# Optimization experiments

Measured on AMD Instinct MI355X. Metric: run time of the kernel, lower is better.

The kernel has to match this reference:

```python
import jax, jax.numpy as jnp
import numpy as np

B, C, N = 8, 256, 1024
D, DK, DV, H, NB = 256, 16, 32, 8, 4
P = N + 1


def layernorm(x, g, b, eps=1e-5):
    m = x.mean(-1, keepdims=True)
    v = x.var(-1, keepdims=True)
    return (x - m) / jnp.sqrt(v + eps) * g + b


def bn_inf(x, g, b, mean, var, eps=1e-5):
    # x: [B, C', N]; stats over channel dim
    scale = (g / jnp.sqrt(var + eps))[None, :, None]
    shift = (b - mean * g / jnp.sqrt(var + eps))[None, :, None]
    return x * scale + shift


def softmax_with_policy(attn, policy, eps=1e-6):
    # attn: [B,H,P,P], policy: [B,P,1]
    n = attn.shape[-1]
    ap = policy.reshape(policy.shape[0], 1, 1, n)
    eye = jnp.eye(n, dtype=ap.dtype)[None, None]
    ap = ap + (1.0 - ap) * eye
    m = attn.max(-1, keepdims=True)
    e = jnp.exp(attn - m) * ap
    return (e + eps / n) / (e.sum(-1, keepdims=True) + eps)


def setup_inputs() -> dict:
    key = jax.random.key(0)
    ks = jax.random.split(key, 24)
    s = 0.02
    inp = {
        'x': jax.random.normal(ks[0], (B, C, N), jnp.float32),
        'policy': jnp.ones((B, P, 1), jnp.float32),
        'conv1_w': jax.random.normal(ks[1], (D, C), jnp.float32) * s,
        'conv2_w': jax.random.normal(ks[2], (D, D), jnp.float32) * s,
        'bn1_g': jnp.ones((D,), jnp.float32),
        'bn1_b': jnp.zeros((D,), jnp.float32),
        'bn1_m': jax.random.normal(ks[3], (D,), jnp.float32) * s,
        'bn1_v': jax.random.uniform(ks[4], (D,), jnp.float32, 0.5, 1.5),
        'bn2_g': jnp.ones((D,), jnp.float32),
        'bn2_b': jnp.zeros((D,), jnp.float32),
        'bn2_m': jax.random.normal(ks[5], (D,), jnp.float32) * s,
        'bn2_v': jax.random.uniform(ks[6], (D,), jnp.float32, 0.5, 1.5),
        'cls_token': jax.random.normal(ks[7], (D,), jnp.float32),
        'ln1_g': jnp.ones((NB, D), jnp.float32),
        'ln1_b': jnp.zeros((NB, D), jnp.float32),
        'ln2_g': jnp.ones((NB, D), jnp.float32),
        'ln2_b': jnp.zeros((NB, D), jnp.float32),
        'wq': jax.random.normal(ks[8], (NB, H * DK, D), jnp.float32) * np.sqrt(2.0 / (D + DK)).astype(np.float32),
        'wk': jax.random.normal(ks[9], (NB, H * DK, D), jnp.float32) * np.sqrt(2.0 / (D + DK)).astype(np.float32),
        'wv': jax.random.normal(ks[10], (NB, H * DV, D), jnp.float32) * np.sqrt(2.0 / (D + DV)).astype(np.float32),
        'fc_w': jax.random.normal(ks[11], (NB, D, H * DV), jnp.float32) * s,
        'ff_w1': jax.random.normal(ks[12], (NB, 2 * D, D), jnp.float32) * s,
        'ff_b1': jnp.zeros((NB, 2 * D), jnp.float32),
        'ff_w2': jax.random.normal(ks[13], (NB, D, 2 * D), jnp.float32) * s,
        'ff_b2': jnp.zeros((NB, D), jnp.float32),
    }
    return inp


def reference(x, policy, conv1_w, conv2_w, bn1_g, bn1_b, bn1_m, bn1_v,
              bn2_g, bn2_b, bn2_m, bn2_v, cls_token,
              ln1_g, ln1_b, ln2_g, ln2_b, wq, wk, wv, fc_w,
              ff_w1, ff_b1, ff_w2, ff_b2):
    # stem: 1x1 conv + BN(inference) + ReLU, twice. x: [B, C, N]
    h = jax.nn.relu(bn_inf(jnp.einsum('dc,bcn->bdn', conv1_w, x), bn1_g, bn1_b, bn1_m, bn1_v))
    h = jax.nn.relu(bn_inf(jnp.einsum('dc,bcn->bdn', conv2_w, h), bn2_g, bn2_b, bn2_m, bn2_v))
    h = h.transpose(0, 2, 1)  # [B, N, D]
    cls = jnp.broadcast_to(cls_token[None, None, :], (B, 1, D))
    h = jnp.concatenate([cls, h], axis=1)  # [B, P, D]

    scale = 1.0 / np.sqrt(DK).astype(np.float32)
    for i in range(NB):
        # attention
        y = layernorm(h, ln1_g[i], ln1_b[i])
        q = jnp.einsum('bnd,ed->bne', y, wq[i]).reshape(B, P, H, DK).transpose(0, 2, 1, 3)
        k = jnp.einsum('bnd,ed->bne', y, wk[i]).reshape(B, P, H, DK).transpose(0, 2, 1, 3)
        v = jnp.einsum('bnd,ed->bne', y, wv[i]).reshape(B, P, H, DV).transpose(0, 2, 1, 3)
        attn = jnp.einsum('bhlk,bhtk->bhlt', q, k) * scale
        attn = softmax_with_policy(attn, policy)
        o = jnp.einsum('bhlt,bhtv->bhlv', attn, v)  # [B,H,P,DV]
        o = o.transpose(0, 2, 1, 3).reshape(B, P, H * DV)
        h = h + jnp.einsum('bne,de->bnd', o, fc_w[i])
        # feed-forward
        y = layernorm(h, ln2_g[i], ln2_b[i])
        y = jax.nn.gelu(jnp.einsum('bnd,ed->bne', y, ff_w1[i]) + ff_b1[i], approximate=False)
        h = h + jnp.einsum('bne,de->bnd', y, ff_w2[i]) + ff_b2[i]
    return h
```

## Files before the change

kernel.cpp:

```cpp
#include <hip/hip_runtime.h>
#include <stdint.h>


typedef unsigned short u16;
typedef unsigned int   u32;
typedef __bf16 bf16x8 __attribute__((ext_vector_type(8)));
typedef float  f32x4  __attribute__((ext_vector_type(4)));
typedef float  f32x16 __attribute__((ext_vector_type(16)));
typedef u32    u32x4  __attribute__((ext_vector_type(4)));

#define DEV static __device__ __forceinline__

DEV float b2f(u16 h){ u32 u = ((u32)h) << 16; return __builtin_bit_cast(float, u); }
DEV u16 f2b(float f){ u32 u = __builtin_bit_cast(u32, f); u32 r = (u + 0x7fffu + ((u >> 16) & 1u)) >> 16; return (u16)r; }
DEV float gelu_f(float x){ return 0.5f * x * (1.0f + erff(x * 0.7071067811865475f)); }
DEV u32 cvtpk(float lo, float hi){
  u32 w;
  asm("v_cvt_pk_bf16_f32 %0, %1, %2" : "=v"(w) : "v"(lo), "v"(hi));
  return w;
}
DEV float exp2_(float x){ float r; asm("v_exp_f32 %0, %1" : "=v"(r) : "v"(x)); return r; }

typedef void __attribute__((address_space(1)))* gas_t;
typedef void __attribute__((address_space(3)))* las_t;
DEV void cp16(const void* g, void* l){
  __builtin_amdgcn_global_load_lds((gas_t)(uintptr_t)g, (las_t)(uintptr_t)l, 16, 0, 0);
}

struct Seg { const float* src; u16* dst; int n; int period; int dstride; int block0; float scale; };
struct SegPack { Seg s[8]; };

__global__ __launch_bounds__(256) void k_convert(SegPack p){
  int bid = blockIdx.x;
  int si = 0;
  #pragma unroll
  for (int i = 1; i < 8; i++) if (bid >= p.s[i].block0) si = i;
  const Seg sg = p.s[si];
  int e0 = (bid - sg.block0) * 2048 + threadIdx.x * 8;
  #pragma unroll
  for (int k = 0; k < 8; k++){
    int e = e0 + k;
    if (e < sg.n) sg.dst[(e / sg.period) * sg.dstride + (e % sg.period)] = f2b(sg.src[e] * sg.scale);
  }
}

__global__ __launch_bounds__(256) void k_transpose_x(const float* __restrict__ x, u16* __restrict__ xT){
  __shared__ float t[32][33];
  int b = blockIdx.z, ct = blockIdx.y, nt = blockIdx.x;
  int tx = threadIdx.x & 31, ty = threadIdx.x >> 5;
  const float* xp = x + ((size_t)b * 256 + ct * 32) * 1024 + nt * 32;
  #pragma unroll
  for (int k = 0; k < 4; k++) t[ty + 8*k][tx] = xp[(size_t)(ty + 8*k) * 1024 + tx];
  __syncthreads();
  u16* op = xT + ((size_t)b * 1024 + nt * 32) * 256 + ct * 32;
  #pragma unroll
  for (int k = 0; k < 4; k++) op[(size_t)(ty + 8*k) * 256 + tx] = f2b(t[tx][ty + 8*k]);
}

__global__ void k_cls(const float* __restrict__ cls, float* __restrict__ h){
  int d = threadIdx.x;
  #pragma unroll
  for (int b = 0; b < 8; b++) h[(size_t)b * 1025 * 256 + d] = cls[d];
}

__global__ __launch_bounds__(256) void k_ln(const float* __restrict__ h, const float* __restrict__ g,
                                            const float* __restrict__ bt, u16* __restrict__ y){
  int lane = threadIdx.x & 63, wv = threadIdx.x >> 6;
  long t = (long)blockIdx.x * 4 + wv;
  if (t >= 8200) return;
  const float* row = h + t * 256;
  float4 v = *reinterpret_cast<const float4*>(row + lane * 4);
  float s = v.x + v.y + v.z + v.w;
  float q = v.x*v.x + v.y*v.y + v.z*v.z + v.w*v.w;
  #pragma unroll
  for (int o = 32; o > 0; o >>= 1){ s += __shfl_xor(s, o); q += __shfl_xor(q, o); }
  float mean = s * (1.f/256.f);
  float var  = q * (1.f/256.f) - mean * mean;
  float rs = rsqrtf(var + 1e-5f);
  ushort4 ov;
  const float* vp = &v.x;
  u16* o16 = (u16*)&ov;
  #pragma unroll
  for (int j = 0; j < 4; j++){
    int c = lane * 4 + j;
    o16[j] = f2b((vp[j] - mean) * rs * g[c] + bt[c]);
  }
  *reinterpret_cast<ushort4*>(y + t * 256 + lane * 4) = ov;
}

template<int EPI, int BM, int BN>
__global__ __launch_bounds__(256) void k_gemmT(const u16* __restrict__ A, const u16* __restrict__ W,
    int M, int K, int E, float* __restrict__ outF, u16* __restrict__ outB,
    u16* __restrict__ outK,
    const float* __restrict__ a0, const float* __restrict__ a1,
    const float* __restrict__ a2, const float* __restrict__ a3){
  constexpr int MR = BM / 32, NR = BN / 32;
  __shared__ __align__(16) u16 As[BM * 64];
  __shared__ __align__(16) u16 Bs[BN * 64];
  const int MTILES = (M + BM - 1) / BM;
  const int MT8 = (MTILES + 7) >> 3;
  const int bid = blockIdx.x;
  const int xcd = bid & 7, rest = bid >> 3;
  const int mi = xcd + 8 * (rest % MT8);
  const int ni = rest / MT8;
  if (mi >= MTILES) return;
  const int tM = mi * BM, tN = ni * BN;
  const int tid = threadIdx.x;
  const int lane = tid & 63, wv = tid >> 6;
  const int wr = wv >> 1, wc = wv & 1;
  f32x4 acc[MR][NR];
  #pragma unroll
  for (int m = 0; m < MR; m++)
    #pragma unroll
    for (int n = 0; n < NR; n++)
      #pragma unroll
      for (int j = 0; j < 4; j++) acc[m][n][j] = 0.f;

  const int l8 = lane >> 3, lm = lane & 7;
  for (int k0 = 0; k0 < K; k0 += 64){
    __syncthreads();
    #pragma unroll
    for (int is = 0; is < BM / 32; is++){
      int row = is * 32 + wv * 8 + l8;
      int kg = lm ^ (row & 7);
      int ra = tM + row; ra = ra < M ? ra : M - 1;
      cp16(A + (size_t)ra * K + k0 + kg * 8, As + is * 2048 + wv * 512);
    }
    #pragma unroll
    for (int is = 0; is < BN / 32; is++){
      int row = is * 32 + wv * 8 + l8;
      int kg = lm ^ (row & 7);
      cp16(W + (size_t)(tN + row) * K + k0 + kg * 8, Bs + is * 2048 + wv * 512);
    }
    __syncthreads();
    #pragma unroll
    for (int kk = 0; kk < 2; kk++){
      bf16x8 af[MR], bfv[NR];
      #pragma unroll
      for (int m = 0; m < MR; m++){
        int row = wr * (BM/2) + m * 16 + (lane & 15);
        int kg = (kk * 4 + (lane >> 4)) ^ (row & 7);
        af[m] = *reinterpret_cast<const bf16x8*>(&As[row * 64 + kg * 8]);
      }
      #pragma unroll
      for (int n = 0; n < NR; n++){
        int row = wc * (BN/2) + n * 16 + (lane & 15);
        int kg = (kk * 4 + (lane >> 4)) ^ (row & 7);
        bfv[n] = *reinterpret_cast<const bf16x8*>(&Bs[row * 64 + kg * 8]);
      }
      #pragma unroll
      for (int m = 0; m < MR; m++)
        #pragma unroll
        for (int n = 0; n < NR; n++)
          acc[m][n] = __builtin_amdgcn_mfma_f32_16x16x32_bf16(af[m], bfv[n], acc[m][n], 0, 0, 0);
    }
  }
  #pragma unroll
  for (int n = 0; n < NR; n++){
    const int col = tN + wc * (BN/2) + n * 16 + (lane & 15);
    float scale = 0.f, shift = 0.f, bias = 0.f;
    if (EPI == 1 || EPI == 2){
      float gv = a0[col], bv = a1[col], mv = a2[col], vv = a3[col];
      scale = gv * rsqrtf(vv + 1e-5f);
      shift = bv - mv * scale;
    }
    if (EPI == 4 || EPI == 5) bias = a0[col];
    #pragma unroll
    for (int m = 0; m < MR; m++){
      const int row0 = tM + wr * (BM/2) + m * 16 + ((lane >> 4) << 2);
      #pragma unroll
      for (int j = 0; j < 4; j++){
        int r = row0 + j;
        if (r < M){
          float v = acc[m][n][j];
          if (EPI == 1){ v = v * scale + shift; v = v > 0.f ? v : 0.f; outB[(size_t)r * E + col] = f2b(v); }
          else if (EPI == 2){ v = v * scale + shift; v = v > 0.f ? v : 0.f; outF[(size_t)(r + (r >> 10) + 1) * 256 + col] = v; }
          else if (EPI == 3){ outF[(size_t)r * E + col] += v; }
          else if (EPI == 4){ outB[(size_t)r * E + col] = f2b(gelu_f(v + bias)); }
          else if (EPI == 5){ outF[(size_t)r * E + col] += v + bias; }
          else {
            int bb = r / 1025, tok = r - bb * 1025;
            if (col < 128){
              outB[(size_t)r * 512 + col] = f2b(v);
            } else if (col < 256){
              int hk = (col - 128) >> 4, dk = col & 15;
              outK[((size_t)((bb * 8 + hk) * 1032 + tok)) * 16 + dk] = f2b(v);
            } else {
              u16 bv = f2b(v);
              outB[(size_t)r * 512 + col] = bv;
              u16* vt = (u16*)outF;
              int hv = (col - 256) >> 5, dv = (col - 256) & 31;
              vt[((size_t)((bb * 8 + hv) * 32 + dv)) * 1032 + tok] = bv;
            }
          }
        }
      }
    }
  }
}

__global__ __launch_bounds__(256) void k_attn(const u16* __restrict__ qkv,
    const u16* __restrict__ kb, const u16* __restrict__ vt,
    const float* __restrict__ pol, u16* __restrict__ o){
  __shared__ float pol_s[1088];
  __shared__ float oB[3][32][33];
  __shared__ float lsB[3][32];
  const int tid = threadIdx.x;
  const int lane = tid & 63, wv = tid >> 6;
  const int l32 = lane & 31, hi = lane >> 5;
  const int bid = blockIdx.x;
  const int xcd = bid & 7, idx = bid >> 3;
  const int bh = xcd * 8 + idx / 33, qt = idx % 33;
  const int b = bh >> 3, hh = bh & 7;
  const size_t rowbase = (size_t)b * 1025;
  const u16* kbh = kb + (size_t)bh * 1032 * 16;
  const int qg = qt * 32 + l32;
  const int qr = qg > 1024 ? 1024 : qg;
  const bf16x8 qf = *reinterpret_cast<const bf16x8*>(qkv + (rowbase + qr) * 512 + hh * 16 + hi * 8);
  float sqq = 0.f, scl = 0.f;
  {
    const bf16x8 kown = *reinterpret_cast<const bf16x8*>(kbh + (size_t)qr * 16 + hi * 8);
    const bf16x8 kcls = *reinterpret_cast<const bf16x8*>(kbh + (size_t)1024 * 16 + hi * 8);
    #pragma unroll
    for (int i = 0; i < 8; i++){
      sqq += (float)qf[i] * (float)kown[i];
      scl += (float)qf[i] * (float)kcls[i];
    }
    sqq += __shfl_xor(sqq, 32);
    scl += __shfl_xor(scl, 32);
  }
  const u16* vrow = vt + ((size_t)(bh * 32 + l32)) * 1032;
  const u16* krow = kbh + (size_t)((wv * 256) + l32) * 16 + hi * 8;
  for (int t = tid; t < 1088; t += 256){
    float p = (t <= 1024) ? pol[rowbase + t] : 0.f;
    pol_s[t] = (p > 0.f) ? __log2f(p) : -1.0e30f;
  }
  __syncthreads();

  float ls = 0.f;
  f32x16 oacc;
  #pragma unroll
  for (int r = 0; r < 16; r++) oacc[r] = 0.f;

  bf16x8 ka = *reinterpret_cast<const bf16x8*>(krow);
  #pragma unroll
  for (int s8 = 0; s8 < 8; s8++){
    const int jb32 = wv * 256 + s8 * 32;
    const bf16x8 ka_cur = ka;
    if (s8 < 7) ka = *reinterpret_cast<const bf16x8*>(krow + (size_t)(s8 + 1) * 512);
    const bf16x8 va0 = *reinterpret_cast<const bf16x8*>(vrow + jb32 + hi * 8);
    const bf16x8 va1 = *reinterpret_cast<const bf16x8*>(vrow + jb32 + 16 + hi * 8);
    f32x16 fz;
    #pragma unroll
    for (int r = 0; r < 16; r++) fz[r] = 0.f;
    f32x16 st = __builtin_amdgcn_mfma_f32_32x32x16_bf16(ka_cur, qf, fz, 0, 0, 0);
    float e[16];
    #pragma unroll
    for (int r = 0; r < 16; r++){
      int jg2 = jb32 + (r & 3) + 8 * (r >> 2) + 4 * hi;
      e[r] = exp2_(st[r] + pol_s[jg2]);
    }
    float s01 = (e[0] + e[1]) + (e[2] + e[3]);
    float s23 = (e[4] + e[5]) + (e[6] + e[7]);
    float s45 = (e[8] + e[9]) + (e[10] + e[11]);
    float s67 = (e[12] + e[13]) + (e[14] + e[15]);
    float psum = (s01 + s23) + (s45 + s67);
    psum += __shfl_xor(psum, 32);
    ls += psum;
    #pragma unroll
    for (int c = 0; c < 2; c++){
      u32 A0 = cvtpk(e[c*8+0], e[c*8+1]);
      u32 A1 = cvtpk(e[c*8+2], e[c*8+3]);
      u32 B0 = cvtpk(e[c*8+4], e[c*8+5]);
      u32 B1 = cvtpk(e[c*8+6], e[c*8+7]);
      u32 pA0 = __shfl_xor(A0, 32), pB0 = __shfl_xor(B0, 32);
      u32 pA1 = __shfl_xor(A1, 32), pB1 = __shfl_xor(B1, 32);
      u32x4 pw;
      pw.x = hi ? pB0 : A0;
      pw.y = hi ? pB1 : A1;
      pw.z = hi ? B0 : pA0;
      pw.w = hi ? B1 : pA1;
      bf16x8 pb = __builtin_bit_cast(bf16x8, pw);
      oacc = __builtin_amdgcn_mfma_f32_32x32x16_bf16(c == 0 ? va0 : va1, pb, oacc, 0, 0, 0);
    }
  }
  __syncthreads();
  if (wv > 0){
    lsB[wv-1][l32] = ls;
    #pragma unroll
    for (int r = 0; r < 16; r++) oB[wv-1][l32][(r & 3) + 8 * (r >> 2) + 4 * hi] = oacc[r];
  }
  __syncthreads();
  if (wv == 0 && qg <= 1024){
    float ls_t = (ls + lsB[0][l32]) + (lsB[1][l32] + lsB[2][l32]);
    const float pq = exp2_(pol_s[qg]);
    const float ec = (1.f - pq) * exp2_(sqq);
    const float ecl = exp2_(scl + pol_s[1024]);
    ls_t += ec + ecl;
    const float inv = 1.f / (ls_t + 1e-6f);
    u16* orow = o + (rowbase + qg) * 256 + hh * 32;
    const u16* vq   = qkv + (rowbase + qg) * 512 + 256 + hh * 32;
    const u16* vcls = qkv + (rowbase + 1024) * 512 + 256 + hh * 32;
    #pragma unroll
    for (int rq = 0; rq < 4; rq++){
      const int dv0 = 8 * rq + 4 * hi;
      const ushort4 vv4 = *reinterpret_cast<const ushort4*>(vq + dv0);
      const ushort4 vc4 = *reinterpret_cast<const ushort4*>(vcls + dv0);
      const u16* vv = (const u16*)&vv4;
      const u16* vc = (const u16*)&vc4;
      uint2 wout;
      u32* wp = &wout.x;
      #pragma unroll
      for (int j2 = 0; j2 < 2; j2++){
        const int d0 = dv0 + j2 * 2;
        float v0 = (oacc[rq*4 + j2*2    ] + oB[0][l32][d0    ] + oB[1][l32][d0    ] + oB[2][l32][d0    ]
                    + ec * b2f(vv[j2*2    ]) + ecl * b2f(vc[j2*2    ])) * inv;
        float v1 = (oacc[rq*4 + j2*2 + 1] + oB[0][l32][d0 + 1] + oB[1][l32][d0 + 1] + oB[2][l32][d0 + 1]
                    + ec * b2f(vv[j2*2 + 1]) + ecl * b2f(vc[j2*2 + 1])) * inv;
        wp[j2] = ((u32)f2b(v1) << 16) | (u32)f2b(v0);
      }
      *reinterpret_cast<uint2*>(orow + dv0) = wout;
    }
  }
}

extern "C" void kernel_launch(void* const* d_in, const int* in_sizes, int n_in,
                              void* d_out, int out_size, void* d_ws, size_t ws_size,
                              hipStream_t stream){
  const float* x    = (const float*)d_in[0];
  const float* pol  = (const float*)d_in[1];
  const float* c1w  = (const float*)d_in[2];
  const float* c2w  = (const float*)d_in[3];
  const float* bn1g = (const float*)d_in[4];
  const float* bn1b = (const float*)d_in[5];
  const float* bn1m = (const float*)d_in[6];
  const float* bn1v = (const float*)d_in[7];
  const float* bn2g = (const float*)d_in[8];
  const float* bn2b = (const float*)d_in[9];
  const float* bn2m = (const float*)d_in[10];
  const float* bn2v = (const float*)d_in[11];
  const float* cls  = (const float*)d_in[12];
  const float* ln1g = (const float*)d_in[13];
  const float* ln1b = (const float*)d_in[14];
  const float* ln2g = (const float*)d_in[15];
  const float* ln2b = (const float*)d_in[16];
  const float* wq   = (const float*)d_in[17];
  const float* wk   = (const float*)d_in[18];
  const float* wvp  = (const float*)d_in[19];
  const float* fcw  = (const float*)d_in[20];
  const float* ffw1 = (const float*)d_in[21];
  const float* ffb1 = (const float*)d_in[22];
  const float* ffw2 = (const float*)d_in[23];
  const float* ffb2 = (const float*)d_in[24];
  float* h = (float*)d_out;

  u16* ws   = (u16*)d_ws;
  u16* wc1  = ws;
  u16* wc2  = wc1  + 65536;
  u16* wqkv = wc2  + 65536;
  u16* wfc  = wqkv + 524288;
  u16* wff1 = wfc  + 262144;
  u16* wff2 = wff1 + 524288;
  u16* xT   = wff2 + 524288;
  u16* h1   = xT   + 2097152;
  u16* yb   = h1   + 2097152;
  u16* qkvb = yb   + 2099200;
  u16* ob   = qkvb + 4198400;
  u16* vtb  = ob   + 2099200;
  u16* kbb  = vtb  + 2117632;
  u16* ub   = qkvb;

  const float QSCALE = 0.25f * 1.4426950408889634f;
  SegPack sp;
  int b0 = 0;
  sp.s[0] = Seg{ c1w,  wc1,          65536,  65536,  0,      b0, 1.f }; b0 += 32;
  sp.s[1] = Seg{ c2w,  wc2,          65536,  65536,  0,      b0, 1.f }; b0 += 32;
  sp.s[2] = Seg{ wq,   wqkv,         131072, 32768,  131072, b0, QSCALE }; b0 += 64;
  sp.s[3] = Seg{ wk,   wqkv + 32768, 131072, 32768,  131072, b0, 1.f }; b0 += 64;
  sp.s[4] = Seg{ wvp,  wqkv + 65536, 262144, 65536,  131072, b0, 1.f }; b0 += 128;
  sp.s[5] = Seg{ fcw,  wfc,          262144, 262144, 0,      b0, 1.f }; b0 += 128;
  sp.s[6] = Seg{ ffw1, wff1,         524288, 524288, 0,      b0, 1.f }; b0 += 256;
  sp.s[7] = Seg{ ffw2, wff2,         524288, 524288, 0,      b0, 1.f }; b0 += 256;

  k_convert<<<b0, 256, 0, stream>>>(sp);
  k_transpose_x<<<dim3(32, 8, 8), 256, 0, stream>>>(x, xT);
  k_cls<<<1, 256, 0, stream>>>(cls, h);
  k_gemmT<1,64,64><<<8*16*4, 256, 0, stream>>>(xT, wc1, 8192, 256, 256, nullptr, h1, nullptr,
                                               bn1g, bn1b, bn1m, bn1v);
  k_gemmT<2,64,64><<<8*16*4, 256, 0, stream>>>(h1, wc2, 8192, 256, 256, h, nullptr, nullptr,
                                               bn2g, bn2b, bn2m, bn2v);
  for (int i = 0; i < 4; i++){
    k_ln<<<2050, 256, 0, stream>>>(h, ln1g + i*256, ln1b + i*256, yb);
    k_gemmT<6,64,128><<<8*17*4, 256, 0, stream>>>(yb, wqkv + i*131072, 8200, 256, 512,
                                                  (float*)vtb, qkvb, kbb,
                                                  nullptr, nullptr, nullptr, nullptr);
    k_attn<<<2112, 256, 0, stream>>>(qkvb, kbb, vtb, pol, ob);
    k_gemmT<3,64,64><<<8*17*4, 256, 0, stream>>>(ob, wfc + i*65536, 8200, 256, 256, h, nullptr, nullptr,
                                                 nullptr, nullptr, nullptr, nullptr);
    k_ln<<<2050, 256, 0, stream>>>(h, ln2g + i*256, ln2b + i*256, yb);
    k_gemmT<4,64,128><<<8*17*4, 256, 0, stream>>>(yb, wff1 + i*131072, 8200, 256, 512, nullptr, ub, nullptr,
                                                  ffb1 + i*512, nullptr, nullptr, nullptr);
    k_gemmT<5,64,64><<<8*17*4, 256, 0, stream>>>(ub, wff2 + i*131072, 8200, 512, 256, h, nullptr, nullptr,
                                                 ffb2 + i*256, nullptr, nullptr, nullptr);
  }
}
```

Before: 354.8 us.

## Fuse layernorm into the QKV and FF1 GEMM prologues

Removes the standalone layernorm kernel. A new GEMM kernel loads the whole 64x256 fp32 activation tile, normalises it in registers, and stores it once as bf16 in a swizzled LDS tile before the K loop. Only the weight tiles are then streamed. This drops eight launches and the bf16 y round-trip through global memory. In exchange, each N-tile block (four per row tile) recomputes the layernorm and rereads fp32 h, and the larger LDS footprint may reduce occupancy.

```diff
diff --git a/kernel.cpp b/kernel.cpp
--- a/kernel.cpp
+++ b/kernel.cpp
@@ -63,35 +63,9 @@
   for (int b = 0; b < 8; b++) h[(size_t)b * 1025 * 256 + d] = cls[d];
 }
 
-__global__ __launch_bounds__(256) void k_ln(const float* __restrict__ h, const float* __restrict__ g,
-                                            const float* __restrict__ bt, u16* __restrict__ y){
-  int lane = threadIdx.x & 63, wv = threadIdx.x >> 6;
-  long t = (long)blockIdx.x * 4 + wv;
-  if (t >= 8200) return;
-  const float* row = h + t * 256;
-  float4 v = *reinterpret_cast<const float4*>(row + lane * 4);
-  float s = v.x + v.y + v.z + v.w;
-  float q = v.x*v.x + v.y*v.y + v.z*v.z + v.w*v.w;
-  #pragma unroll
-  for (int o = 32; o > 0; o >>= 1){ s += __shfl_xor(s, o); q += __shfl_xor(q, o); }
-  float mean = s * (1.f/256.f);
-  float var  = q * (1.f/256.f) - mean * mean;
-  float rs = rsqrtf(var + 1e-5f);
-  ushort4 ov;
-  const float* vp = &v.x;
-  u16* o16 = (u16*)&ov;
-  #pragma unroll
-  for (int j = 0; j < 4; j++){
-    int c = lane * 4 + j;
-    o16[j] = f2b((vp[j] - mean) * rs * g[c] + bt[c]);
-  }
-  *reinterpret_cast<ushort4*>(y + t * 256 + lane * 4) = ov;
-}
-
 template<int EPI, int BM, int BN>
 __global__ __launch_bounds__(256) void k_gemmT(const u16* __restrict__ A, const u16* __restrict__ W,
     int M, int K, int E, float* __restrict__ outF, u16* __restrict__ outB,
-    u16* __restrict__ outK,
     const float* __restrict__ a0, const float* __restrict__ a1,
     const float* __restrict__ a2, const float* __restrict__ a3){
   constexpr int MR = BM / 32, NR = BN / 32;
@@ -164,7 +138,7 @@
       scale = gv * rsqrtf(vv + 1e-5f);
       shift = bv - mv * scale;
     }
-    if (EPI == 4 || EPI == 5) bias = a0[col];
+    if (EPI == 5) bias = a0[col];
     #pragma unroll
     for (int m = 0; m < MR; m++){
       const int row0 = tM + wr * (BM/2) + m * 16 + ((lane >> 4) << 2);
@@ -176,8 +150,126 @@
           if (EPI == 1){ v = v * scale + shift; v = v > 0.f ? v : 0.f; outB[(size_t)r * E + col] = f2b(v); }
           else if (EPI == 2){ v = v * scale + shift; v = v > 0.f ? v : 0.f; outF[(size_t)(r + (r >> 10) + 1) * 256 + col] = v; }
           else if (EPI == 3){ outF[(size_t)r * E + col] += v; }
-          else if (EPI == 4){ outB[(size_t)r * E + col] = f2b(gelu_f(v + bias)); }
-          else if (EPI == 5){ outF[(size_t)r * E + col] += v + bias; }
+          else { outF[(size_t)r * E + col] += v + bias; }
+        }
+      }
+    }
+  }
+}
+
+template<int EPI>
+__global__ __launch_bounds__(256) void k_gln(const float* __restrict__ hA, const u16* __restrict__ W,
+    int M, int E, const float* __restrict__ lg, const float* __restrict__ lb,
+    float* __restrict__ outF, u16* __restrict__ outB, u16* __restrict__ outK,
+    const float* __restrict__ a0){
+  constexpr int BM = 64, BN = 128, MR = 2, NR = 4;
+  __shared__ __align__(16) u16 As[64 * 256];
+  __shared__ __align__(16) u16 Bs[BN * 64];
+  const int MTILES = (M + BM - 1) / BM;
+  const int MT8 = (MTILES + 7) >> 3;
+  const int bid = blockIdx.x;
+  const int xcd = bid & 7, rest = bid >> 3;
+  const int mi = xcd + 8 * (rest % MT8);
+  const int ni = rest / MT8;
+  if (mi >= MTILES) return;
+  const int tM = mi * BM, tN = ni * BN;
+  const int tid = threadIdx.x;
+  const int lane = tid & 63, wv = tid >> 6;
+  const int wr = wv >> 1, wc = wv & 1;
+
+  {
+    const int r = tid >> 2, qd = tid & 3;
+    int ra = tM + r; ra = ra < M ? ra : M - 1;
+    const float* hrow = hA + (size_t)ra * 256 + qd * 64;
+    float4 hv[16];
+    #pragma unroll
+    for (int c = 0; c < 16; c++) hv[c] = *reinterpret_cast<const float4*>(hrow + c * 4);
+    float s = 0.f, q = 0.f;
+    #pragma unroll
+    for (int c = 0; c < 16; c++){
+      s += (hv[c].x + hv[c].y) + (hv[c].z + hv[c].w);
+      q += (hv[c].x*hv[c].x + hv[c].y*hv[c].y) + (hv[c].z*hv[c].z + hv[c].w*hv[c].w);
+    }
+    s += __shfl_xor(s, 1); s += __shfl_xor(s, 2);
+    q += __shfl_xor(q, 1); q += __shfl_xor(q, 2);
+    const float mean = s * (1.f/256.f);
+    const float var  = q * (1.f/256.f) - mean * mean;
+    const float rs = rsqrtf(var + 1e-5f);
+    #pragma unroll
+    for (int w = 0; w < 8; w++){
+      u32x4 d;
+      #pragma unroll
+      for (int half = 0; half < 2; half++){
+        const int c = 2 * w + half;
+        const float4 g4 = *reinterpret_cast<const float4*>(lg + qd * 64 + c * 4);
+        const float4 b4 = *reinterpret_cast<const float4*>(lb + qd * 64 + c * 4);
+        float v0 = (hv[c].x - mean) * rs * g4.x + b4.x;
+        float v1 = (hv[c].y - mean) * rs * g4.y + b4.y;
+        float v2 = (hv[c].z - mean) * rs * g4.z + b4.z;
+        float v3 = (hv[c].w - mean) * rs * g4.w + b4.w;
+        d[half*2 + 0] = cvtpk(v0, v1);
+        d[half*2 + 1] = cvtpk(v2, v3);
+      }
+      const int gL = (qd * 8 + w) ^ (r & 7);
+      *reinterpret_cast<u32x4*>(&As[r * 256 + gL * 8]) = d;
+    }
+  }
+
+  f32x4 acc[MR][NR];
+  #pragma unroll
+  for (int m = 0; m < MR; m++)
+    #pragma unroll
+    for (int n = 0; n < NR; n++)
+      #pragma unroll
+      for (int j = 0; j < 4; j++) acc[m][n][j] = 0.f;
+
+  const int l8 = lane >> 3, lm = lane & 7;
+  for (int k0 = 0; k0 < 256; k0 += 64){
+    __syncthreads();
+    #pragma unroll
+    for (int is = 0; is < NR; is++){
+      int row = is * 32 + wv * 8 + l8;
+      int kg = lm ^ (row & 7);
+      cp16(W + (size_t)(tN + row) * 256 + k0 + kg * 8, Bs + is * 2048 + wv * 512);
+    }
+    __syncthreads();
+    #pragma unroll
+    for (int kk = 0; kk < 2; kk++){
+      bf16x8 af[MR], bfv[NR];
+      #pragma unroll
+      for (int m = 0; m < MR; m++){
+        int row = wr * 32 + m * 16 + (lane & 15);
+        int gk = (k0 >> 3) + kk * 4 + (lane >> 4);
+        int g = gk ^ (row & 7);
+        af[m] = *reinterpret_cast<const bf16x8*>(&As[row * 256 + g * 8]);
+      }
+      #pragma unroll
+      for (int n = 0; n < NR; n++){
+        int row = wc * 64 + n * 16 + (lane & 15);
+        int kg = (kk * 4 + (lane >> 4)) ^ (row & 7);
+        bfv[n] = *reinterpret_cast<const bf16x8*>(&Bs[row * 64 + kg * 8]);
+      }
+      #pragma unroll
+      for (int m = 0; m < MR; m++)
+        #pragma unroll
+        for (int n = 0; n < NR; n++)
+          acc[m][n] = __builtin_amdgcn_mfma_f32_16x16x32_bf16(af[m], bfv[n], acc[m][n], 0, 0, 0);
+    }
+  }
+  #pragma unroll
+  for (int n = 0; n < NR; n++){
+    const int col = tN + wc * 64 + n * 16 + (lane & 15);
+    float bias = 0.f;
+    if (EPI == 4) bias = a0[col];
+    #pragma unroll
+    for (int m = 0; m < MR; m++){
+      const int row0 = tM + wr * 32 + m * 16 + ((lane >> 4) << 2);
+      #pragma unroll
+      for (int j = 0; j < 4; j++){
+        int r = row0 + j;
+        if (r < M){
+          float v = acc[m][n][j];
+          if (EPI == 4){ outB[(size_t)r * E + col] = f2b(gelu_f(v + bias)); }
           else {
             int bb = r / 1025, tok = r - bb * 1025;
             if (col < 128){
@@ -363,8 +455,7 @@
   u16* wff2 = wff1 + 524288;
   u16* xT   = wff2 + 524288;
   u16* h1   = xT   + 2097152;
-  u16* yb   = h1   + 2097152;
-  u16* qkvb = yb   + 2099200;
+  u16* qkvb = h1   + 2097152;
   u16* ob   = qkvb + 4198400;
   u16* vtb  = ob   + 2099200;
   u16* kbb  = vtb  + 2117632;
@@ -385,22 +476,21 @@
   k_convert<<<b0, 256, 0, stream>>>(sp);
   k_transpose_x<<<dim3(32, 8, 8), 256, 0, stream>>>(x, xT);
   k_cls<<<1, 256, 0, stream>>>(cls, h);
-  k_gemmT<1,64,64><<<8*16*4, 256, 0, stream>>>(xT, wc1, 8192, 256, 256, nullptr, h1, nullptr,
+  k_gemmT<1,64,64><<<8*16*4, 256, 0, stream>>>(xT, wc1, 8192, 256, 256, nullptr, h1,
                                                bn1g, bn1b, bn1m, bn1v);
-  k_gemmT<2,64,64><<<8*16*4, 256, 0, stream>>>(h1, wc2, 8192, 256, 256, h, nullptr, nullptr,
+  k_gemmT<2,64,64><<<8*16*4, 256, 0, stream>>>(h1, wc2, 8192, 256, 256, h, nullptr,
                                                bn2g, bn2b, bn2m, bn2v);
   for (int i = 0; i < 4; i++){
-    k_ln<<<2050, 256, 0, stream>>>(h, ln1g + i*256, ln1b + i*256, yb);
-    k_gemmT<6,64,128><<<8*17*4, 256, 0, stream>>>(yb, wqkv + i*131072, 8200, 256, 512,
-                                                  (float*)vtb, qkvb, kbb,
-                                                  nullptr, nullptr, nullptr, nullptr);
+    k_gln<6><<<8*17*4, 256, 0, stream>>>(h, wqkv + i*131072, 8200, 512,
+                                         ln1g + i*256, ln1b + i*256,
+                                         (float*)vtb, qkvb, kbb, nullptr);
     k_attn<<<2112, 256, 0, stream>>>(qkvb, kbb, vtb, pol, ob);
-    k_gemmT<3,64,64><<<8*17*4, 256, 0, stream>>>(ob, wfc + i*65536, 8200, 256, 256, h, nullptr, nullptr,
+    k_gemmT<3,64,64><<<8*17*4, 256, 0, stream>>>(ob, wfc + i*65536, 8200, 256, 256, h, nullptr,
                                                  nullptr, nullptr, nullptr, nullptr);
-    k_ln<<<2050, 256, 0, stream>>>(h, ln2g + i*256, ln2b + i*256, yb);
-    k_gemmT<4,64,128><<<8*17*4, 256, 0, stream>>>(yb, wff1 + i*131072, 8200, 256, 512, nullptr, ub, nullptr,
-                                                  ffb1 + i*512, nullptr, nullptr, nullptr);
-    k_gemmT<5,64,64><<<8*17*4, 256, 0, stream>>>(ub, wff2 + i*131072, 8200, 512, 256, h, nullptr, nullptr,
+    k_gln<4><<<8*17*4, 256, 0, stream>>>(h, wff1 + i*131072, 8200, 512,
+                                         ln2g + i*256, ln2b + i*256,
+                                         nullptr, ub, nullptr, ffb1 + i*512);
+    k_gemmT<5,64,64><<<8*17*4, 256, 0, stream>>>(ub, wff2 + i*131072, 8200, 512, 256, h, nullptr,
                                                  ffb2 + i*256, nullptr, nullptr, nullptr);
   }
 }
```

Measured after the change: 453.8 us. 1.28x slower.
